# Optimization experiments

Hardware: AMD Instinct MI355X
Metric: run time of the kernel (lower is better)

The kernel has to match this reference:

```python
import jax, jax.numpy as jnp
import numpy as np

B, S, D, H = 4, 2048, 1024, 16
HD = D // H  # head_dim = 64


def setup_inputs() -> dict:
    key = jax.random.key(0)
    ks = jax.random.split(key, 9)
    sd = 1.0 / np.sqrt(D)
    x = jax.random.normal(ks[0], (B, S, D), dtype=jnp.float32)
    Wq = jax.random.normal(ks[1], (D, D), dtype=jnp.float32) * sd
    Wk = jax.random.normal(ks[2], (D, D), dtype=jnp.float32) * sd
    Wv = jax.random.normal(ks[3], (D, D), dtype=jnp.float32) * sd
    Wo = jax.random.normal(ks[4], (D, D), dtype=jnp.float32) * sd
    bq = jax.random.normal(ks[5], (D,), dtype=jnp.float32) * sd
    bk = jax.random.normal(ks[6], (D,), dtype=jnp.float32) * sd
    bv = jax.random.normal(ks[7], (D,), dtype=jnp.float32) * sd
    bo = jax.random.normal(ks[8], (D,), dtype=jnp.float32) * sd
    return {"x": x, "Wq": Wq, "bq": bq, "Wk": Wk, "bk": bk,
            "Wv": Wv, "bv": bv, "Wo": Wo, "bo": bo}


def reference(x, Wq, bq, Wk, bk, Wv, bv, Wo, bo):
    b, s, d = x.shape
    scale = jnp.float32(np.sqrt(HD))
    # projections, split into heads: (b, h, s, hd)
    def heads(y):
        return y.reshape(b, s, H, HD).transpose(0, 2, 1, 3)
    Q = heads(x @ Wq + bq)
    K = heads(x @ Wk + bk)
    V = heads(x @ Wv + bv)
    # (b, h, s, s) scores with causal mask
    scores = jnp.einsum('bhqd,bhkd->bhqk', Q, K) / scale
    causal = jnp.tril(jnp.ones((s, s), dtype=bool))
    scores = jnp.where(causal[None, None], scores, jnp.float32(-jnp.inf))
    probs = jax.nn.softmax(scores, axis=-1)
    out = jnp.einsum('bhqk,bhkd->bhqd', probs, V)
    out = out.transpose(0, 2, 1, 3).reshape(b, s, d)
    return out @ Wo + bo
```

## Files before the change

### kernel.cpp

```cpp
#include <hip/hip_runtime.h>
#include <hip/hip_bf16.h>
#include <cstdint>

typedef __bf16 bf16x8 __attribute__((ext_vector_type(8)));
typedef float f32x4 __attribute__((ext_vector_type(4)));
typedef float f32x16 __attribute__((ext_vector_type(16)));
typedef unsigned short u16t;

__device__ __forceinline__ u16t f2bf(float f) {
    uint32_t u = __builtin_bit_cast(uint32_t, f);
    u += 0x7FFF + ((u >> 16) & 1);
    return (u16t)(u >> 16);
}

constexpr int Bb = 4, Ss = 2048, Dd = 1024, Hh = 16;
constexpr int Mrows = Bb * Ss;
constexpr float NEG = -1e30f;
constexpr float QSCALE = 0.125f * 1.44269504088896340736f;

__global__ __launch_bounds__(256) void cvt_bf16(const float* __restrict__ in,
                                                u16t* __restrict__ out, int n) {
    int i = (blockIdx.x * 256 + threadIdx.x) * 4;
    if (i >= n) return;
    float4 v = *(const float4*)(in + i);
    u16t o[4] = {f2bf(v.x), f2bf(v.y), f2bf(v.z), f2bf(v.w)};
    *(ushort4*)(out + i) = *(ushort4*)o;
}

__global__ __launch_bounds__(256) void transpose_cvt4(const float* __restrict__ W0,
                                                      const float* __restrict__ W1,
                                                      const float* __restrict__ W2,
                                                      const float* __restrict__ W3,
                                                      u16t* __restrict__ Tqkv,
                                                      u16t* __restrict__ To) {
    __shared__ float tile[64][65];
    int z = blockIdx.z;
    const float* W = z == 0 ? W0 : z == 1 ? W1 : z == 2 ? W2 : W3;
    u16t* WT = z < 3 ? Tqkv + (size_t)z * Dd * Dd : To;
    int n0 = blockIdx.x * 64, k0 = blockIdx.y * 64;
    int c = threadIdx.x & 63, r0 = (threadIdx.x >> 6) * 16;
    for (int i = 0; i < 16; i++)
        tile[c][r0 + i] = W[(size_t)(k0 + r0 + i) * Dd + n0 + c];
    __syncthreads();
    for (int i = 0; i < 16; i++)
        WT[(size_t)(n0 + r0 + i) * Dd + k0 + c] = f2bf(tile[r0 + i][c]);
}

__global__ __launch_bounds__(256) void gemm_qkv(const u16t* __restrict__ A,
                                                const u16t* __restrict__ BT,
                                                const float* __restrict__ bq,
                                                const float* __restrict__ bk,
                                                const float* __restrict__ bvv,
                                                u16t* __restrict__ Qh,
                                                u16t* __restrict__ Kh,
                                                u16t* __restrict__ Vt) {
    __shared__ __align__(16) u16t Asm[128 * 32];
    __shared__ __align__(16) u16t Bsm[128 * 32];
    int tid = threadIdx.x, lane = tid & 63, w = tid >> 6;
    int wm = w >> 1, wn = w & 1;
    int ln = lane & 15, g = lane >> 4;
    int bid = blockIdx.x;
    int wg = (bid & 7) * 192 + (bid >> 3);
    int n0 = (wg % 24) * 128, m0 = (wg / 24) * 128;

    f32x4 acc[4][4] = {};

    int sr = w * 32 + (lane >> 2);
    int sc = (((lane & 3) ^ (sr & 3)) * 8);
    const u16t* Ag0 = A + (size_t)(m0 + sr) * Dd + sc;
    const u16t* Ag1 = A + (size_t)(m0 + sr + 16) * Dd + sc;
    const u16t* Bg0 = BT + (size_t)(n0 + sr) * Dd + sc;
    const u16t* Bg1 = BT + (size_t)(n0 + sr + 16) * Dd + sc;
    u16t* As0 = &Asm[(w * 32) * 32];
    u16t* As1 = &Asm[(w * 32 + 16) * 32];
    u16t* Bs0 = &Bsm[(w * 32) * 32];
    u16t* Bs1 = &Bsm[(w * 32 + 16) * 32];

    for (int k0 = 0; k0 < Dd; k0 += 32) {
        __syncthreads();
        __builtin_amdgcn_global_load_lds(Ag0 + k0, As0, 16, 0, 0);
        __builtin_amdgcn_global_load_lds(Ag1 + k0, As1, 16, 0, 0);
        __builtin_amdgcn_global_load_lds(Bg0 + k0, Bs0, 16, 0, 0);
        __builtin_amdgcn_global_load_lds(Bg1 + k0, Bs1, 16, 0, 0);
        __syncthreads();
        bf16x8 af[4], bf[4];
        #pragma unroll
        for (int i = 0; i < 4; i++) {
            int row = wm * 64 + i * 16 + ln;
            af[i] = *(const bf16x8*)&Asm[row * 32 + ((g ^ (row & 3)) * 8)];
        }
        #pragma unroll
        for (int j = 0; j < 4; j++) {
            int row = wn * 64 + j * 16 + ln;
            bf[j] = *(const bf16x8*)&Bsm[row * 32 + ((g ^ (row & 3)) * 8)];
        }
        #pragma unroll
        for (int i = 0; i < 4; i++)
            #pragma unroll
            for (int j = 0; j < 4; j++)
                acc[i][j] = __builtin_amdgcn_mfma_f32_16x16x32_bf16(af[i], bf[j], acc[i][j], 0, 0, 0);
    }

    #pragma unroll
    for (int i = 0; i < 4; i++) {
        #pragma unroll
        for (int j = 0; j < 4; j++) {
            int col = n0 + wn * 64 + j * 16 + ln;
            int seg = col >> 10, c1k = col & 1023;
            float bias = seg == 0 ? bq[c1k] : seg == 1 ? bk[c1k] : bvv[c1k];
            int rowb = m0 + wm * 64 + i * 16 + g * 4;
            int b = rowb >> 11, s = rowb & 2047, h = c1k >> 6, hd = c1k & 63;
            if (seg == 0) {
                for (int r = 0; r < 4; r++) {
                    float v = (acc[i][j][r] + bias) * QSCALE;
                    Qh[((size_t)(b * Hh + h) * Ss + s + r) * 64 + hd] = f2bf(v);
                }
            } else if (seg == 1) {
                for (int r = 0; r < 4; r++)
                    Kh[((size_t)(b * Hh + h) * Ss + s + r) * 64 + hd] = f2bf(acc[i][j][r] + bias);
            } else {
                u16t pk4[4];
                for (int r = 0; r < 4; r++) pk4[r] = f2bf(acc[i][j][r] + bias);
                *(ushort4*)(Vt + ((size_t)((b * Hh + h) * 64 + hd) << 11) + s) = *(ushort4*)pk4;
            }
        }
    }
}

__global__ __launch_bounds__(256) void gemm_o(const u16t* __restrict__ A,
                                              const u16t* __restrict__ BT,
                                              const float* __restrict__ bias,
                                              float* __restrict__ outF) {
    __shared__ __align__(16) u16t Asm[128 * 32];
    __shared__ __align__(16) u16t Bsm[128 * 32];
    int tid = threadIdx.x, lane = tid & 63, w = tid >> 6;
    int wm = w >> 1, wn = w & 1;
    int ln = lane & 15, g = lane >> 4;
    int bid = blockIdx.x;
    int wg = (bid & 7) * 64 + (bid >> 3);
    int n0 = (wg & 7) * 128, m0 = (wg >> 3) * 128;

    f32x4 acc[4][4] = {};

    int sr = w * 32 + (lane >> 2);
    int sc = (((lane & 3) ^ (sr & 3)) * 8);
    const u16t* Ag0 = A + (size_t)(m0 + sr) * Dd + sc;
    const u16t* Ag1 = A + (size_t)(m0 + sr + 16) * Dd + sc;
    const u16t* Bg0 = BT + (size_t)(n0 + sr) * Dd + sc;
    const u16t* Bg1 = BT + (size_t)(n0 + sr + 16) * Dd + sc;
    u16t* As0 = &Asm[(w * 32) * 32];
    u16t* As1 = &Asm[(w * 32 + 16) * 32];
    u16t* Bs0 = &Bsm[(w * 32) * 32];
    u16t* Bs1 = &Bsm[(w * 32 + 16) * 32];

    for (int k0 = 0; k0 < Dd; k0 += 32) {
        __syncthreads();
        __builtin_amdgcn_global_load_lds(Ag0 + k0, As0, 16, 0, 0);
        __builtin_amdgcn_global_load_lds(Ag1 + k0, As1, 16, 0, 0);
        __builtin_amdgcn_global_load_lds(Bg0 + k0, Bs0, 16, 0, 0);
        __builtin_amdgcn_global_load_lds(Bg1 + k0, Bs1, 16, 0, 0);
        __syncthreads();
        bf16x8 af[4], bf[4];
        #pragma unroll
        for (int i = 0; i < 4; i++) {
            int row = wm * 64 + i * 16 + ln;
            af[i] = *(const bf16x8*)&Asm[row * 32 + ((g ^ (row & 3)) * 8)];
        }
        #pragma unroll
        for (int j = 0; j < 4; j++) {
            int row = wn * 64 + j * 16 + ln;
            bf[j] = *(const bf16x8*)&Bsm[row * 32 + ((g ^ (row & 3)) * 8)];
        }
        #pragma unroll
        for (int i = 0; i < 4; i++)
            #pragma unroll
            for (int j = 0; j < 4; j++)
                acc[i][j] = __builtin_amdgcn_mfma_f32_16x16x32_bf16(af[i], bf[j], acc[i][j], 0, 0, 0);
    }

    #pragma unroll
    for (int i = 0; i < 4; i++) {
        #pragma unroll
        for (int j = 0; j < 4; j++) {
            int col = n0 + wn * 64 + j * 16 + ln;
            float bv = bias[col];
            int rowb = m0 + wm * 64 + i * 16 + g * 4;
            for (int r = 0; r < 4; r++)
                outF[(size_t)(rowb + r) * Dd + col] = acc[i][j][r] + bv;
        }
    }
}

__global__ __launch_bounds__(256) void attn(const u16t* __restrict__ Qh,
                                            const u16t* __restrict__ Kh,
                                            const u16t* __restrict__ Vt,
                                            u16t* __restrict__ Ob) {
    __shared__ __align__(16) u16t Ksm[2][64 * 64];
    __shared__ __align__(16) u16t Vsm[2][64 * 64];

    int tid = threadIdx.x, lane = tid & 63, w = tid >> 6;
    int l31 = lane & 31, hi = lane >> 5;
    int flat = blockIdx.y * 8 + blockIdx.x;
    int xcd = flat & 7, jj = flat >> 3;
    int bh = xcd * 8 + (jj >> 3);
    int ip = jj & 7;

    const u16t* Kb = Kh + (size_t)bh * Ss * 64;
    const u16t* Vb = Vt + (size_t)bh * 64 * Ss;

    int sr0 = w * 16 + (lane >> 3);
    int sr1 = sr0 + 8;
    int sc0 = (((lane & 7) ^ (sr0 & 7) ^ ((sr0 >> 3) & 3)) * 8);
    int sc1 = (((lane & 7) ^ (sr1 & 7) ^ ((sr1 >> 3) & 3)) * 8);
    const u16t* Kg0 = Kb + (size_t)sr0 * 64 + sc0;
    const u16t* Kg1 = Kb + (size_t)sr1 * 64 + sc1;
    const u16t* Vg0 = Vb + (size_t)sr0 * Ss + sc0;
    const u16t* Vg1 = Vb + (size_t)sr1 * Ss + sc1;

    auto stage = [&](int buf, int t) {
        size_t koff = (size_t)t * 64 * 64;
        size_t voff = (size_t)t * 64;
        __builtin_amdgcn_global_load_lds(Kg0 + koff, &Ksm[buf][(w * 2 + 0) * 512], 16, 0, 0);
        __builtin_amdgcn_global_load_lds(Kg1 + koff, &Ksm[buf][(w * 2 + 1) * 512], 16, 0, 0);
        __builtin_amdgcn_global_load_lds(Vg0 + voff, &Vsm[buf][(w * 2 + 0) * 512], 16, 0, 0);
        __builtin_amdgcn_global_load_lds(Vg1 + voff, &Vsm[buf][(w * 2 + 1) * 512], 16, 0, 0);
    };

    int swzr = (l31 & 7) ^ ((l31 >> 3) & 3);

    for (int task = 0; task < 2; task++) {
        int qx = task == 0 ? ip : 15 - ip;
        int qb = qx * 128;
        int q0w = qb + w * 32;
        int qlane = q0w + l31;

        bf16x8 qB[4];
        {
            const u16t* Qp = Qh + ((size_t)bh * Ss + qlane) * 64 + hi * 8;
            #pragma unroll
            for (int ks = 0; ks < 4; ks++)
                qB[ks] = *(const bf16x8*)(Qp + 16 * ks);
        }

        f32x16 oacc[2] = {};
        float m_run = NEG, l_run = 0.f;
        int nt = (qb >> 6) + 2;

        stage(0, 0);
        __syncthreads();

        for (int t = 0; t < nt; t++) {
            int cur = t & 1;
            int kv0 = t << 6;
            if (t + 1 < nt) stage(cur ^ 1, t + 1);

            bool active = (kv0 <= q0w + 31);
            if (active) {
                f32x16 p0 = {}, p1 = {};
                __builtin_amdgcn_s_setprio(1);
                #pragma unroll
                for (int ks = 0; ks < 4; ks++) {
                    int cc = (2 * ks + hi) ^ swzr;
                    bf16x8 ka0 = *(const bf16x8*)&Ksm[cur][(size_t)l31 * 64 + cc * 8];
                    bf16x8 ka1 = *(const bf16x8*)&Ksm[cur][(size_t)(32 + l31) * 64 + cc * 8];
                    p0 = __builtin_amdgcn_mfma_f32_32x32x16_bf16(ka0, qB[ks], p0, 0, 0, 0);
                    p1 = __builtin_amdgcn_mfma_f32_32x32x16_bf16(ka1, qB[ks], p1, 0, 0, 0);
                }
                __builtin_amdgcn_s_setprio(0);

                if (kv0 + 63 > q0w) {
                    #pragma unroll
                    for (int r = 0; r < 16; r++) {
                        int kvg = kv0 + (r & 3) + 8 * (r >> 2) + 4 * hi;
                        if (kvg > qlane)      p0[r] = NEG;
                        if (kvg + 32 > qlane) p1[r] = NEG;
                    }
                }

                float ma = fmaxf(p0[0], p1[0]), mb = fmaxf(p0[1], p1[1]);
                float mc = fmaxf(p0[2], p1[2]), md = fmaxf(p0[3], p1[3]);
                #pragma unroll
                for (int r = 4; r < 16; r += 4) {
                    ma = fmaxf(ma, fmaxf(p0[r], p1[r]));
                    mb = fmaxf(mb, fmaxf(p0[r + 1], p1[r + 1]));
                    mc = fmaxf(mc, fmaxf(p0[r + 2], p1[r + 2]));
                    md = fmaxf(md, fmaxf(p0[r + 3], p1[r + 3]));
                }
                float mt = fmaxf(fmaxf(ma, mb), fmaxf(mc, md));
                mt = fmaxf(mt, __shfl_xor(mt, 32));
                if (__any(mt > m_run + 10.0f)) {
                    float mn = fmaxf(m_run, mt);
                    float al = __builtin_exp2f(m_run - mn);
                    m_run = mn;
                    l_run *= al;
                    #pragma unroll
                    for (int r = 0; r < 16; r++) { oacc[0][r] *= al; oacc[1][r] *= al; }
                }
                #pragma unroll
                for (int r = 0; r < 16; r++) {
                    p0[r] = __builtin_exp2f(p0[r] - m_run);
                    p1[r] = __builtin_exp2f(p1[r] - m_run);
                }
                float sa = 0.f, sb = 0.f, sc2 = 0.f, sd = 0.f;
                #pragma unroll
                for (int r = 0; r < 16; r += 4) {
                    sa += p0[r] + p1[r];
                    sb += p0[r + 1] + p1[r + 1];
                    sc2 += p0[r + 2] + p1[r + 2];
                    sd += p0[r + 3] + p1[r + 3];
                }
                float rsum = (sa + sb) + (sc2 + sd);
                rsum += __shfl_xor(rsum, 32);
                l_run += rsum;

                bf16x8 pb[4];
                {
                    uint32_t c0, c1, c2, c3;
                    asm("v_cvt_pk_bf16_f32 %0, %1, %2" : "=v"(c0) : "v"(p0[0]), "v"(p0[1]));
                    asm("v_cvt_pk_bf16_f32 %0, %1, %2" : "=v"(c1) : "v"(p0[2]), "v"(p0[3]));
                    asm("v_cvt_pk_bf16_f32 %0, %1, %2" : "=v"(c2) : "v"(p0[4]), "v"(p0[5]));
                    asm("v_cvt_pk_bf16_f32 %0, %1, %2" : "=v"(c3) : "v"(p0[6]), "v"(p0[7]));
                    asm volatile("v_permlane32_swap_b32 %0, %1" : "+v"(c0), "+v"(c2));
                    asm volatile("v_permlane32_swap_b32 %0, %1" : "+v"(c1), "+v"(c3));
                    uint32_t w4[4] = {c0, c1, c2, c3};
                    pb[0] = *(bf16x8*)w4;
                    uint32_t d0, d1, d2, d3;
                    asm("v_cvt_pk_bf16_f32 %0, %1, %2" : "=v"(d0) : "v"(p0[8]),  "v"(p0[9]));
                    asm("v_cvt_pk_bf16_f32 %0, %1, %2" : "=v"(d1) : "v"(p0[10]), "v"(p0[11]));
                    asm("v_cvt_pk_bf16_f32 %0, %1, %2" : "=v"(d2) : "v"(p0[12]), "v"(p0[13]));
                    asm("v_cvt_pk_bf16_f32 %0, %1, %2" : "=v"(d3) : "v"(p0[14]), "v"(p0[15]));
                    asm volatile("v_permlane32_swap_b32 %0, %1" : "+v"(d0), "+v"(d2));
                    asm volatile("v_permlane32_swap_b32 %0, %1" : "+v"(d1), "+v"(d3));
                    uint32_t w5[4] = {d0, d1, d2, d3};
                    pb[1] = *(bf16x8*)w5;
                    uint32_t e0, e1, e2, e3;
                    asm("v_cvt_pk_bf16_f32 %0, %1, %2" : "=v"(e0) : "v"(p1[0]), "v"(p1[1]));
                    asm("v_cvt_pk_bf16_f32 %0, %1, %2" : "=v"(e1) : "v"(p1[2]), "v"(p1[3]));
                    asm("v_cvt_pk_bf16_f32 %0, %1, %2" : "=v"(e2) : "v"(p1[4]), "v"(p1[5]));
                    asm("v_cvt_pk_bf16_f32 %0, %1, %2" : "=v"(e3) : "v"(p1[6]), "v"(p1[7]));
                    asm volatile("v_permlane32_swap_b32 %0, %1" : "+v"(e0), "+v"(e2));
                    asm volatile("v_permlane32_swap_b32 %0, %1" : "+v"(e1), "+v"(e3));
                    uint32_t w6[4] = {e0, e1, e2, e3};
                    pb[2] = *(bf16x8*)w6;
                    uint32_t f0, f1, f2, f3;
                    asm("v_cvt_pk_bf16_f32 %0, %1, %2" : "=v"(f0) : "v"(p1[8]),  "v"(p1[9]));
                    asm("v_cvt_pk_bf16_f32 %0, %1, %2" : "=v"(f1) : "v"(p1[10]), "v"(p1[11]));
                    asm("v_cvt_pk_bf16_f32 %0, %1, %2" : "=v"(f2) : "v"(p1[12]), "v"(p1[13]));
                    asm("v_cvt_pk_bf16_f32 %0, %1, %2" : "=v"(f3) : "v"(p1[14]), "v"(p1[15]));
                    asm volatile("v_permlane32_swap_b32 %0, %1" : "+v"(f0), "+v"(f2));
                    asm volatile("v_permlane32_swap_b32 %0, %1" : "+v"(f1), "+v"(f3));
                    uint32_t w7[4] = {f0, f1, f2, f3};
                    pb[3] = *(bf16x8*)w7;
                }

                __builtin_amdgcn_s_setprio(1);
                #pragma unroll
                for (int dt = 0; dt < 2; dt++) {
                    int drow = dt * 32 + l31;
                    #pragma unroll
                    for (int ks = 0; ks < 4; ks++) {
                        int cc = (2 * ks + hi) ^ swzr;
                        bf16x8 va = *(const bf16x8*)&Vsm[cur][(size_t)drow * 64 + cc * 8];
                        oacc[dt] = __builtin_amdgcn_mfma_f32_32x32x16_bf16(va, pb[ks], oacc[dt], 0, 0, 0);
                    }
                }
                __builtin_amdgcn_s_setprio(0);
            }
            __syncthreads();
        }

        float inv = 1.0f / l_run;
        int b = bh >> 4, h = bh & 15;
        u16t* Op = Ob + ((size_t)(b * Ss + qlane)) * Dd + h * 64;
        #pragma unroll
        for (int dt = 0; dt < 2; dt++)
            #pragma unroll
            for (int rq = 0; rq < 4; rq++) {
                u16t pk4[4];
                #pragma unroll
                for (int j = 0; j < 4; j++) pk4[j] = f2bf(oacc[dt][rq * 4 + j] * inv);
                int d0 = dt * 32 + rq * 8 + hi * 4;
                *(ushort4*)(Op + d0) = *(ushort4*)pk4;
            }
    }
}

extern "C" void kernel_launch(void* const* d_in, const int* in_sizes, int n_in,
                              void* d_out, int out_size, void* d_ws, size_t ws_size,
                              hipStream_t stream) {
    const float* x  = (const float*)d_in[0];
    const float* Wq = (const float*)d_in[1];
    const float* bq = (const float*)d_in[2];
    const float* Wk = (const float*)d_in[3];
    const float* bk = (const float*)d_in[4];
    const float* Wv = (const float*)d_in[5];
    const float* bv = (const float*)d_in[6];
    const float* Wo = (const float*)d_in[7];
    const float* bo = (const float*)d_in[8];

    char* ws = (char*)d_ws;
    size_t off = 0;
    auto alloc = [&](size_t bytes) { char* p = ws + off; off += (bytes + 255) & ~(size_t)255; return p; };
    u16t* xb    = (u16t*)alloc((size_t)Mrows * Dd * 2);
    u16t* WqkvT = (u16t*)alloc((size_t)3 * Dd * Dd * 2);
    u16t* WoT   = (u16t*)alloc((size_t)Dd * Dd * 2);
    u16t* Qh    = (u16t*)alloc((size_t)Mrows * Dd * 2);
    u16t* Kh    = (u16t*)alloc((size_t)Mrows * Dd * 2);
    u16t* Vtp   = (u16t*)alloc((size_t)Mrows * Dd * 2);
    u16t* Ob    = (u16t*)alloc((size_t)Mrows * Dd * 2);

    int nx = Mrows * Dd;
    cvt_bf16<<<nx / (256 * 4), 256, 0, stream>>>(x, xb, nx);
    dim3 tg(16, 16, 4);
    transpose_cvt4<<<tg, 256, 0, stream>>>(Wq, Wk, Wv, Wo, WqkvT, WoT);

    gemm_qkv<<<1536, 256, 0, stream>>>(xb, WqkvT, bq, bk, bv, Qh, Kh, Vtp);

    dim3 ga(8, Bb * Hh);
    attn<<<ga, 256, 0, stream>>>(Qh, Kh, Vtp, Ob);

    gemm_o<<<512, 256, 0, stream>>>(Ob, WoT, bo, (float*)d_out);
}
```

Measured before the change: 208.4 us.

## Process paired causal query tiles in one KV sweep sharing staged K/V

Each block used to handle its two query tiles (ip and 15-ip) one after the other, loading K/V tiles from global memory for each pass. Now both tiles are processed in a single loop over KV tiles, so every staged K/V tile in LDS serves both query tiles, and the early-tile task skips once it passes its causal limit. The pairing index is also mirrored for half of the blocks to change the XCD/L2 access order. In exchange, two sets of Q fragments and accumulators stay live at once, which raises register pressure and may lower occupancy or cause spills.

```diff
diff --git a/kernel.cpp b/kernel.cpp
--- a/kernel.cpp
+++ b/kernel.cpp
@@ -203,7 +203,9 @@
     int flat = blockIdx.y * 8 + blockIdx.x;
     int xcd = flat & 7, jj = flat >> 3;
     int bh = xcd * 8 + (jj >> 3);
-    int ip = jj & 7;
+    int ipb = jj & 7;
+    int ip = ((jj >> 5) & 1) ? 7 - ipb : ipb;
+    int qxA = ip, qxB = 15 - ip;
 
     const u16t* Kb = Kh + (size_t)bh * Ss * 64;
     const u16t* Vb = Vt + (size_t)bh * 64 * Ss;
@@ -228,157 +230,174 @@
 
     int swzr = (l31 & 7) ^ ((l31 >> 3) & 3);
 
-    for (int task = 0; task < 2; task++) {
-        int qx = task == 0 ? ip : 15 - ip;
-        int qb = qx * 128;
-        int q0w = qb + w * 32;
-        int qlane = q0w + l31;
-
-        bf16x8 qB[4];
+    auto body = [&](const bf16x8* qB, float& m_run, float& l_run, f32x16* oacc,
+                    int q0w, int qlane, int kv0, int cur) {
+        f32x16 p0 = {}, p1 = {};
+        __builtin_amdgcn_s_setprio(1);
+        #pragma unroll
+        for (int ks = 0; ks < 4; ks++) {
+            int cc = (2 * ks + hi) ^ swzr;
+            bf16x8 ka0 = *(const bf16x8*)&Ksm[cur][(size_t)l31 * 64 + cc * 8];
+            bf16x8 ka1 = *(const bf16x8*)&Ksm[cur][(size_t)(32 + l31) * 64 + cc * 8];
+            p0 = __builtin_amdgcn_mfma_f32_32x32x16_bf16(ka0, qB[ks], p0, 0, 0, 0);
+            p1 = __builtin_amdgcn_mfma_f32_32x32x16_bf16(ka1, qB[ks], p1, 0, 0, 0);
+        }
+        __builtin_amdgcn_s_setprio(0);
+
+        if (kv0 + 63 > q0w) {
+            #pragma unroll
+            for (int r = 0; r < 16; r++) {
+                int kvg = kv0 + (r & 3) + 8 * (r >> 2) + 4 * hi;
+                if (kvg > qlane)      p0[r] = NEG;
+                if (kvg + 32 > qlane) p1[r] = NEG;
+            }
+        }
+
+        float ma = fmaxf(p0[0], p1[0]), mb = fmaxf(p0[1], p1[1]);
+        float mc = fmaxf(p0[2], p1[2]), md = fmaxf(p0[3], p1[3]);
+        #pragma unroll
+        for (int r = 4; r < 16; r += 4) {
+            ma = fmaxf(ma, fmaxf(p0[r], p1[r]));
+            mb = fmaxf(mb, fmaxf(p0[r + 1], p1[r + 1]));
+            mc = fmaxf(mc, fmaxf(p0[r + 2], p1[r + 2]));
+            md = fmaxf(md, fmaxf(p0[r + 3], p1[r + 3]));
+        }
+        float mt = fmaxf(fmaxf(ma, mb), fmaxf(mc, md));
+        mt = fmaxf(mt, __shfl_xor(mt, 32));
+        if (__any(mt > m_run + 10.0f)) {
+            float mn = fmaxf(m_run, mt);
+            float al = __builtin_exp2f(m_run - mn);
+            m_run = mn;
+            l_run *= al;
+            #pragma unroll
+            for (int r = 0; r < 16; r++) { oacc[0][r] *= al; oacc[1][r] *= al; }
+        }
+        #pragma unroll
+        for (int r = 0; r < 16; r++) {
+            p0[r] = __builtin_exp2f(p0[r] - m_run);
+            p1[r] = __builtin_exp2f(p1[r] - m_run);
+        }
+        float sa = 0.f, sb = 0.f, sc2 = 0.f, sd = 0.f;
+        #pragma unroll
+        for (int r = 0; r < 16; r += 4) {
+            sa += p0[r] + p1[r];
+            sb += p0[r + 1] + p1[r + 1];
+            sc2 += p0[r + 2] + p1[r + 2];
+            sd += p0[r + 3] + p1[r + 3];
+        }
+        float rsum = (sa + sb) + (sc2 + sd);
+        rsum += __shfl_xor(rsum, 32);
+        l_run += rsum;
+
+        bf16x8 pb[4];
         {
-            const u16t* Qp = Qh + ((size_t)bh * Ss + qlane) * 64 + hi * 8;
-            #pragma unroll
-            for (int ks = 0; ks < 4; ks++)
-                qB[ks] = *(const bf16x8*)(Qp + 16 * ks);
-        }
-
-        f32x16 oacc[2] = {};
-        float m_run = NEG, l_run = 0.f;
-        int nt = (qb >> 6) + 2;
-
-        stage(0, 0);
+            uint32_t c0, c1, c2, c3;
+            asm("v_cvt_pk_bf16_f32 %0, %1, %2" : "=v"(c0) : "v"(p0[0]), "v"(p0[1]));
+            asm("v_cvt_pk_bf16_f32 %0, %1, %2" : "=v"(c1) : "v"(p0[2]), "v"(p0[3]));
+            asm("v_cvt_pk_bf16_f32 %0, %1, %2" : "=v"(c2) : "v"(p0[4]), "v"(p0[5]));
+            asm("v_cvt_pk_bf16_f32 %0, %1, %2" : "=v"(c3) : "v"(p0[6]), "v"(p0[7]));
+            asm volatile("v_permlane32_swap_b32 %0, %1" : "+v"(c0), "+v"(c2));
+            asm volatile("v_permlane32_swap_b32 %0, %1" : "+v"(c1), "+v"(c3));
+            uint32_t w4[4] = {c0, c1, c2, c3};
+            pb[0] = *(bf16x8*)w4;
+            uint32_t d0, d1, d2, d3;
+            asm("v_cvt_pk_bf16_f32 %0, %1, %2" : "=v"(d0) : "v"(p0[8]),  "v"(p0[9]));
+            asm("v_cvt_pk_bf16_f32 %0, %1, %2" : "=v"(d1) : "v"(p0[10]), "v"(p0[11]));
+            asm("v_cvt_pk_bf16_f32 %0, %1, %2" : "=v"(d2) : "v"(p0[12]), "v"(p0[13]));
+            asm("v_cvt_pk_bf16_f32 %0, %1, %2" : "=v"(d3) : "v"(p0[14]), "v"(p0[15]));
+            asm volatile("v_permlane32_swap_b32 %0, %1" : "+v"(d0), "+v"(d2));
+            asm volatile("v_permlane32_swap_b32 %0, %1" : "+v"(d1), "+v"(d3));
+            uint32_t w5[4] = {d0, d1, d2, d3};
+            pb[1] = *(bf16x8*)w5;
+            uint32_t e0, e1, e2, e3;
+            asm("v_cvt_pk_bf16_f32 %0, %1, %2" : "=v"(e0) : "v"(p1[0]), "v"(p1[1]));
+            asm("v_cvt_pk_bf16_f32 %0, %1, %2" : "=v"(e1) : "v"(p1[2]), "v"(p1[3]));
+            asm("v_cvt_pk_bf16_f32 %0, %1, %2" : "=v"(e2) : "v"(p1[4]), "v"(p1[5]));
+            asm("v_cvt_pk_bf16_f32 %0, %1, %2" : "=v"(e3) : "v"(p1[6]), "v"(p1[7]));
+            asm volatile("v_permlane32_swap_b32 %0, %1" : "+v"(e0), "+v"(e2));
+            asm volatile("v_permlane32_swap_b32 %0, %1" : "+v"(e1), "+v"(e3));
+            uint32_t w6[4] = {e0, e1, e2, e3};
+            pb[2] = *(bf16x8*)w6;
+            uint32_t f0, f1, f2, f3;
+            asm("v_cvt_pk_bf16_f32 %0, %1, %2" : "=v"(f0) : "v"(p1[8]),  "v"(p1[9]));
+            asm("v_cvt_pk_bf16_f32 %0, %1, %2" : "=v"(f1) : "v"(p1[10]), "v"(p1[11]));
+            asm("v_cvt_pk_bf16_f32 %0, %1, %2" : "=v"(f2) : "v"(p1[12]), "v"(p1[13]));
+            asm("v_cvt_pk_bf16_f32 %0, %1, %2" : "=v"(f3) : "v"(p1[14]), "v"(p1[15]));
+            asm volatile("v_permlane32_swap_b32 %0, %1" : "+v"(f0), "+v"(f2));
+            asm volatile("v_permlane32_swap_b32 %0, %1" : "+v"(f1), "+v"(f3));
+            uint32_t w7[4] = {f0, f1, f2, f3};
+            pb[3] = *(bf16x8*)w7;
+        }
+
+        __builtin_amdgcn_s_setprio(1);
+        #pragma unroll
+        for (int dt = 0; dt < 2; dt++) {
+            int drow = dt * 32 + l31;
+            #pragma unroll
+            for (int ks = 0; ks < 4; ks++) {
+                int cc = (2 * ks + hi) ^ swzr;
+                bf16x8 va = *(const bf16x8*)&Vsm[cur][(size_t)drow * 64 + cc * 8];
+                oacc[dt] = __builtin_amdgcn_mfma_f32_32x32x16_bf16(va, pb[ks], oacc[dt], 0, 0, 0);
+            }
+        }
+        __builtin_amdgcn_s_setprio(0);
+    };
+
+    int q0wA = qxA * 128 + w * 32, qlaneA = q0wA + l31;
+    int q0wB = qxB * 128 + w * 32, qlaneB = q0wB + l31;
+    bf16x8 qBA[4], qBB[4];
+    {
+        const u16t* QpA = Qh + ((size_t)bh * Ss + qlaneA) * 64 + hi * 8;
+        const u16t* QpB = Qh + ((size_t)bh * Ss + qlaneB) * 64 + hi * 8;
+        #pragma unroll
+        for (int ks = 0; ks < 4; ks++) {
+            qBA[ks] = *(const bf16x8*)(QpA + 16 * ks);
+            qBB[ks] = *(const bf16x8*)(QpB + 16 * ks);
+        }
+    }
+    f32x16 oaccA[2] = {}, oaccB[2] = {};
+    float mA = NEG, lA = 0.f, mB = NEG, lB = 0.f;
+
+    int ntB = 2 * qxB + 2;
+
+    stage(0, 0);
+    __syncthreads();
+
+    for (int t = 0; t < ntB; t++) {
+        int cur = t & 1;
+        int kv0 = t << 6;
+        if (t + 1 < ntB) stage(cur ^ 1, t + 1);
+
+        if (kv0 <= q0wA + 31) body(qBA, mA, lA, oaccA, q0wA, qlaneA, kv0, cur);
+        if (kv0 <= q0wB + 31) body(qBB, mB, lB, oaccB, q0wB, qlaneB, kv0, cur);
         __syncthreads();
-
-        for (int t = 0; t < nt; t++) {
-            int cur = t & 1;
-            int kv0 = t << 6;
-            if (t + 1 < nt) stage(cur ^ 1, t + 1);
-
-            bool active = (kv0 <= q0w + 31);
-            if (active) {
-                f32x16 p0 = {}, p1 = {};
-                __builtin_amdgcn_s_setprio(1);
-                #pragma unroll
-                for (int ks = 0; ks < 4; ks++) {
-                    int cc = (2 * ks + hi) ^ swzr;
-                    bf16x8 ka0 = *(const bf16x8*)&Ksm[cur][(size_t)l31 * 64 + cc * 8];
-                    bf16x8 ka1 = *(const bf16x8*)&Ksm[cur][(size_t)(32 + l31) * 64 + cc * 8];
-                    p0 = __builtin_amdgcn_mfma_f32_32x32x16_bf16(ka0, qB[ks], p0, 0, 0, 0);
-                    p1 = __builtin_amdgcn_mfma_f32_32x32x16_bf16(ka1, qB[ks], p1, 0, 0, 0);
-                }
-                __builtin_amdgcn_s_setprio(0);
-
-                if (kv0 + 63 > q0w) {
-                    #pragma unroll
-                    for (int r = 0; r < 16; r++) {
-                        int kvg = kv0 + (r & 3) + 8 * (r >> 2) + 4 * hi;
-                        if (kvg > qlane)      p0[r] = NEG;
-                        if (kvg + 32 > qlane) p1[r] = NEG;
-                    }
-                }
-
-                float ma = fmaxf(p0[0], p1[0]), mb = fmaxf(p0[1], p1[1]);
-                float mc = fmaxf(p0[2], p1[2]), md = fmaxf(p0[3], p1[3]);
-                #pragma unroll
-                for (int r = 4; r < 16; r += 4) {
-                    ma = fmaxf(ma, fmaxf(p0[r], p1[r]));
-                    mb = fmaxf(mb, fmaxf(p0[r + 1], p1[r + 1]));
-                    mc = fmaxf(mc, fmaxf(p0[r + 2], p1[r + 2]));
-                    md = fmaxf(md, fmaxf(p0[r + 3], p1[r + 3]));
-                }
-                float mt = fmaxf(fmaxf(ma, mb), fmaxf(mc, md));
-                mt = fmaxf(mt, __shfl_xor(mt, 32));
-                if (__any(mt > m_run + 10.0f)) {
-                    float mn = fmaxf(m_run, mt);
-                    float al = __builtin_exp2f(m_run - mn);
-                    m_run = mn;
-                    l_run *= al;
-                    #pragma unroll
-                    for (int r = 0; r < 16; r++) { oacc[0][r] *= al; oacc[1][r] *= al; }
-                }
-                #pragma unroll
-                for (int r = 0; r < 16; r++) {
-                    p0[r] = __builtin_exp2f(p0[r] - m_run);
-                    p1[r] = __builtin_exp2f(p1[r] - m_run);
-                }
-                float sa = 0.f, sb = 0.f, sc2 = 0.f, sd = 0.f;
-                #pragma unroll
-                for (int r = 0; r < 16; r += 4) {
-                    sa += p0[r] + p1[r];
-                    sb += p0[r + 1] + p1[r + 1];
-                    sc2 += p0[r + 2] + p1[r + 2];
-                    sd += p0[r + 3] + p1[r + 3];
-                }
-                float rsum = (sa + sb) + (sc2 + sd);
-                rsum += __shfl_xor(rsum, 32);
-                l_run += rsum;
-
-                bf16x8 pb[4];
-                {
-                    uint32_t c0, c1, c2, c3;
-                    asm("v_cvt_pk_bf16_f32 %0, %1, %2" : "=v"(c0) : "v"(p0[0]), "v"(p0[1]));
-                    asm("v_cvt_pk_bf16_f32 %0, %1, %2" : "=v"(c1) : "v"(p0[2]), "v"(p0[3]));
-                    asm("v_cvt_pk_bf16_f32 %0, %1, %2" : "=v"(c2) : "v"(p0[4]), "v"(p0[5]));
-                    asm("v_cvt_pk_bf16_f32 %0, %1, %2" : "=v"(c3) : "v"(p0[6]), "v"(p0[7]));
-                    asm volatile("v_permlane32_swap_b32 %0, %1" : "+v"(c0), "+v"(c2));
-                    asm volatile("v_permlane32_swap_b32 %0, %1" : "+v"(c1), "+v"(c3));
-                    uint32_t w4[4] = {c0, c1, c2, c3};
-                    pb[0] = *(bf16x8*)w4;
-                    uint32_t d0, d1, d2, d3;
-                    asm("v_cvt_pk_bf16_f32 %0, %1, %2" : "=v"(d0) : "v"(p0[8]),  "v"(p0[9]));
-                    asm("v_cvt_pk_bf16_f32 %0, %1, %2" : "=v"(d1) : "v"(p0[10]), "v"(p0[11]));
-                    asm("v_cvt_pk_bf16_f32 %0, %1, %2" : "=v"(d2) : "v"(p0[12]), "v"(p0[13]));
-                    asm("v_cvt_pk_bf16_f32 %0, %1, %2" : "=v"(d3) : "v"(p0[14]), "v"(p0[15]));
-                    asm volatile("v_permlane32_swap_b32 %0, %1" : "+v"(d0), "+v"(d2));
-                    asm volatile("v_permlane32_swap_b32 %0, %1" : "+v"(d1), "+v"(d3));
-                    uint32_t w5[4] = {d0, d1, d2, d3};
-                    pb[1] = *(bf16x8*)w5;
-                    uint32_t e0, e1, e2, e3;
-                    asm("v_cvt_pk_bf16_f32 %0, %1, %2" : "=v"(e0) : "v"(p1[0]), "v"(p1[1]));
-                    asm("v_cvt_pk_bf16_f32 %0, %1, %2" : "=v"(e1) : "v"(p1[2]), "v"(p1[3]));
-                    asm("v_cvt_pk_bf16_f32 %0, %1, %2" : "=v"(e2) : "v"(p1[4]), "v"(p1[5]));
-                    asm("v_cvt_pk_bf16_f32 %0, %1, %2" : "=v"(e3) : "v"(p1[6]), "v"(p1[7]));
-                    asm volatile("v_permlane32_swap_b32 %0, %1" : "+v"(e0), "+v"(e2));
-                    asm volatile("v_permlane32_swap_b32 %0, %1" : "+v"(e1), "+v"(e3));
-                    uint32_t w6[4] = {e0, e1, e2, e3};
-                    pb[2] = *(bf16x8*)w6;
-                    uint32_t f0, f1, f2, f3;
-                    asm("v_cvt_pk_bf16_f32 %0, %1, %2" : "=v"(f0) : "v"(p1[8]),  "v"(p1[9]));
-                    asm("v_cvt_pk_bf16_f32 %0, %1, %2" : "=v"(f1) : "v"(p1[10]), "v"(p1[11]));
-                    asm("v_cvt_pk_bf16_f32 %0, %1, %2" : "=v"(f2) : "v"(p1[12]), "v"(p1[13]));
-                    asm("v_cvt_pk_bf16_f32 %0, %1, %2" : "=v"(f3) : "v"(p1[14]), "v"(p1[15]));
-                    asm volatile("v_permlane32_swap_b32 %0, %1" : "+v"(f0), "+v"(f2));
-                    asm volatile("v_permlane32_swap_b32 %0, %1" : "+v"(f1), "+v"(f3));
-                    uint32_t w7[4] = {f0, f1, f2, f3};
-                    pb[3] = *(bf16x8*)w7;
-                }
-
-                __builtin_amdgcn_s_setprio(1);
-                #pragma unroll
-                for (int dt = 0; dt < 2; dt++) {
-                    int drow = dt * 32 + l31;
-                    #pragma unroll
-                    for (int ks = 0; ks < 4; ks++) {
-                        int cc = (2 * ks + hi) ^ swzr;
-                        bf16x8 va = *(const bf16x8*)&Vsm[cur][(size_t)drow * 64 + cc * 8];
-                        oacc[dt] = __builtin_amdgcn_mfma_f32_32x32x16_bf16(va, pb[ks], oacc[dt], 0, 0, 0);
-                    }
-                }
-                __builtin_amdgcn_s_setprio(0);
-            }
-            __syncthreads();
-        }
-
-        float inv = 1.0f / l_run;
-        int b = bh >> 4, h = bh & 15;
-        u16t* Op = Ob + ((size_t)(b * Ss + qlane)) * Dd + h * 64;
+    }
+
+    int b = bh >> 4, h = bh & 15;
+    {
+        float inv = 1.0f / lA;
+        u16t* Op = Ob + ((size_t)(b * Ss + qlaneA)) * Dd + h * 64;
         #pragma unroll
         for (int dt = 0; dt < 2; dt++)
             #pragma unroll
             for (int rq = 0; rq < 4; rq++) {
                 u16t pk4[4];
                 #pragma unroll
-                for (int j = 0; j < 4; j++) pk4[j] = f2bf(oacc[dt][rq * 4 + j] * inv);
+                for (int j = 0; j < 4; j++) pk4[j] = f2bf(oaccA[dt][rq * 4 + j] * inv);
+                int d0 = dt * 32 + rq * 8 + hi * 4;
+                *(ushort4*)(Op + d0) = *(ushort4*)pk4;
+            }
+    }
+    {
+        float inv = 1.0f / lB;
+        u16t* Op = Ob + ((size_t)(b * Ss + qlaneB)) * Dd + h * 64;
+        #pragma unroll
+        for (int dt = 0; dt < 2; dt++)
+            #pragma unroll
+            for (int rq = 0; rq < 4; rq++) {
+                u16t pk4[4];
+                #pragma unroll
+                for (int j = 0; j < 4; j++) pk4[j] = f2bf(oaccB[dt][rq * 4 + j] * inv);
                 int d0 = dt * 32 + rq * 8 + hi * 4;
                 *(ushort4*)(Op + d0) = *(ushort4*)pk4;
             }
```

Result: slower. 213.0 us (+2.2%).

## Use 128x256 GEMM tiles with 8 waves and triple-buffered async LDS loads

Applied to the files above, without the earlier changes.

Replaces the QKV and output-projection GEMM main loops with a shared macro. Each 512-thread block computes a 128x256 tile with BK=64. The global-to-LDS loads are triple-buffered, using explicit s_barrier and vmcnt waits so the next tiles load while the current one is computed. This aims to hide memory latency and halve the barrier count per K step, at the cost of more LDS per block (about 144KB), which limits occupancy to one block per CU. The hand-counted vmcnt values must match the per-thread load count exactly.

```diff
diff --git a/kernel.cpp b/kernel.cpp
--- a/kernel.cpp
+++ b/kernel.cpp
@@ -46,7 +46,80 @@
         WT[(size_t)(n0 + r0 + i) * Dd + k0 + c] = f2bf(tile[r0 + i][c]);
 }
 
-__global__ __launch_bounds__(256) void gemm_qkv(const u16t* __restrict__ A,
+
+#define GEMM_CORE_512(A_, BT_, m0_, n0_)                                                    \
+    __shared__ __align__(16) u16t Asm3[3][128 * 64];                                        \
+    __shared__ __align__(16) u16t Bsm3[3][256 * 64];                                        \
+    int tid = threadIdx.x, lane = tid & 63, w = tid >> 6;                                   \
+    int wm = w >> 2, wn = w & 3;                                                            \
+    int ln = lane & 15, g = lane >> 4;                                                      \
+    int l3 = lane >> 3, l7 = lane & 7;                                                      \
+    int swz = (l7 ^ (l3 & 7)) * 8;                                                          \
+    const u16t* Ap[2]; int Ao[2];                                                           \
+    _Pragma("unroll")                                                                       \
+    for (int ii = 0; ii < 2; ii++) {                                                        \
+        int rg = m0_ + ii * 64 + w * 8 + l3;                                                \
+        Ap[ii] = A_ + (size_t)rg * Dd + swz;                                                \
+        Ao[ii] = ii * 4096 + w * 512;                                                       \
+    }                                                                                       \
+    const u16t* Bp[4]; int Bo[4];                                                           \
+    _Pragma("unroll")                                                                       \
+    for (int ii = 0; ii < 4; ii++) {                                                        \
+        int rg = n0_ + ii * 64 + w * 8 + l3;                                                \
+        Bp[ii] = BT_ + (size_t)rg * Dd + swz;                                               \
+        Bo[ii] = ii * 4096 + w * 512;                                                       \
+    }                                                                                       \
+    auto stage = [&](int buf, int t) {                                                      \
+        int k0 = t * 64;                                                                    \
+        _Pragma("unroll")                                                                   \
+        for (int ii = 0; ii < 2; ii++)                                                      \
+            __builtin_amdgcn_global_load_lds(Ap[ii] + k0, &Asm3[buf][Ao[ii]], 16, 0, 0);    \
+        _Pragma("unroll")                                                                   \
+        for (int ii = 0; ii < 4; ii++)                                                      \
+            __builtin_amdgcn_global_load_lds(Bp[ii] + k0, &Bsm3[buf][Bo[ii]], 16, 0, 0);    \
+    };                                                                                      \
+    f32x4 acc[4][4] = {};                                                                   \
+    int coff[2] = {((g) ^ (ln & 7)) * 8, ((4 + g) ^ (ln & 7)) * 8};                         \
+    int arow = wm * 64 + ln;                                                                \
+    int brow = wn * 64 + ln;                                                                \
+    auto compute = [&](int buf) {                                                           \
+        bf16x8 af[4][2], bfr[4][2];                                                         \
+        _Pragma("unroll")                                                                   \
+        for (int i = 0; i < 4; i++)                                                         \
+            _Pragma("unroll")                                                               \
+            for (int ks = 0; ks < 2; ks++)                                                  \
+                af[i][ks] = *(const bf16x8*)&Asm3[buf][(arow + i * 16) * 64 + coff[ks]];    \
+        _Pragma("unroll")                                                                   \
+        for (int j = 0; j < 4; j++)                                                         \
+            _Pragma("unroll")                                                               \
+            for (int ks = 0; ks < 2; ks++)                                                  \
+                bfr[j][ks] = *(const bf16x8*)&Bsm3[buf][(brow + j * 16) * 64 + coff[ks]];   \
+        _Pragma("unroll")                                                                   \
+        for (int i = 0; i < 4; i++)                                                         \
+            _Pragma("unroll")                                                               \
+            for (int j = 0; j < 4; j++) {                                                   \
+                acc[i][j] = __builtin_amdgcn_mfma_f32_16x16x32_bf16(af[i][0], bfr[j][0],    \
+                                                                    acc[i][j], 0, 0, 0);    \
+                acc[i][j] = __builtin_amdgcn_mfma_f32_16x16x32_bf16(af[i][1], bfr[j][1],    \
+                                                                    acc[i][j], 0, 0, 0);    \
+            }                                                                               \
+    };                                                                                      \
+    stage(0, 0);                                                                            \
+    stage(1, 1);                                                                            \
+    for (int t = 0; t < 14; t++) {                                                          \
+        asm volatile("s_barrier" ::: "memory");                                             \
+        stage((t + 2) % 3, t + 2);                                                          \
+        asm volatile("s_waitcnt vmcnt(12)" ::: "memory");                                   \
+        compute(t % 3);                                                                     \
+    }                                                                                       \
+    asm volatile("s_barrier" ::: "memory");                                                 \
+    asm volatile("s_waitcnt vmcnt(6)" ::: "memory");                                        \
+    compute(14 % 3);                                                                        \
+    asm volatile("s_barrier" ::: "memory");                                                 \
+    asm volatile("s_waitcnt vmcnt(0)" ::: "memory");                                        \
+    compute(15 % 3);
+
+__global__ __launch_bounds__(512) void gemm_qkv(const u16t* __restrict__ A,
                                                 const u16t* __restrict__ BT,
                                                 const float* __restrict__ bq,
                                                 const float* __restrict__ bk,
@@ -54,52 +127,11 @@
                                                 u16t* __restrict__ Qh,
                                                 u16t* __restrict__ Kh,
                                                 u16t* __restrict__ Vt) {
-    __shared__ __align__(16) u16t Asm[128 * 32];
-    __shared__ __align__(16) u16t Bsm[128 * 32];
-    int tid = threadIdx.x, lane = tid & 63, w = tid >> 6;
-    int wm = w >> 1, wn = w & 1;
-    int ln = lane & 15, g = lane >> 4;
     int bid = blockIdx.x;
-    int wg = (bid & 7) * 192 + (bid >> 3);
-    int n0 = (wg % 24) * 128, m0 = (wg / 24) * 128;
-
-    f32x4 acc[4][4] = {};
-
-    int sr = w * 32 + (lane >> 2);
-    int sc = (((lane & 3) ^ (sr & 3)) * 8);
-    const u16t* Ag0 = A + (size_t)(m0 + sr) * Dd + sc;
-    const u16t* Ag1 = A + (size_t)(m0 + sr + 16) * Dd + sc;
-    const u16t* Bg0 = BT + (size_t)(n0 + sr) * Dd + sc;
-    const u16t* Bg1 = BT + (size_t)(n0 + sr + 16) * Dd + sc;
-    u16t* As0 = &Asm[(w * 32) * 32];
-    u16t* As1 = &Asm[(w * 32 + 16) * 32];
-    u16t* Bs0 = &Bsm[(w * 32) * 32];
-    u16t* Bs1 = &Bsm[(w * 32 + 16) * 32];
-
-    for (int k0 = 0; k0 < Dd; k0 += 32) {
-        __syncthreads();
-        __builtin_amdgcn_global_load_lds(Ag0 + k0, As0, 16, 0, 0);
-        __builtin_amdgcn_global_load_lds(Ag1 + k0, As1, 16, 0, 0);
-        __builtin_amdgcn_global_load_lds(Bg0 + k0, Bs0, 16, 0, 0);
-        __builtin_amdgcn_global_load_lds(Bg1 + k0, Bs1, 16, 0, 0);
-        __syncthreads();
-        bf16x8 af[4], bf[4];
-        #pragma unroll
-        for (int i = 0; i < 4; i++) {
-            int row = wm * 64 + i * 16 + ln;
-            af[i] = *(const bf16x8*)&Asm[row * 32 + ((g ^ (row & 3)) * 8)];
-        }
-        #pragma unroll
-        for (int j = 0; j < 4; j++) {
-            int row = wn * 64 + j * 16 + ln;
-            bf[j] = *(const bf16x8*)&Bsm[row * 32 + ((g ^ (row & 3)) * 8)];
-        }
-        #pragma unroll
-        for (int i = 0; i < 4; i++)
-            #pragma unroll
-            for (int j = 0; j < 4; j++)
-                acc[i][j] = __builtin_amdgcn_mfma_f32_16x16x32_bf16(af[i], bf[j], acc[i][j], 0, 0, 0);
-    }
+    int wg = (bid & 7) * 96 + (bid >> 3);
+    int m0 = (wg / 12) * 128, n0 = (wg % 12) * 256;
+
+    GEMM_CORE_512(A, BT, m0, n0)
 
     #pragma unroll
     for (int i = 0; i < 4; i++) {
@@ -127,56 +159,15 @@
     }
 }
 
-__global__ __launch_bounds__(256) void gemm_o(const u16t* __restrict__ A,
+__global__ __launch_bounds__(512) void gemm_o(const u16t* __restrict__ A,
                                               const u16t* __restrict__ BT,
                                               const float* __restrict__ bias,
                                               float* __restrict__ outF) {
-    __shared__ __align__(16) u16t Asm[128 * 32];
-    __shared__ __align__(16) u16t Bsm[128 * 32];
-    int tid = threadIdx.x, lane = tid & 63, w = tid >> 6;
-    int wm = w >> 1, wn = w & 1;
-    int ln = lane & 15, g = lane >> 4;
     int bid = blockIdx.x;
-    int wg = (bid & 7) * 64 + (bid >> 3);
-    int n0 = (wg & 7) * 128, m0 = (wg >> 3) * 128;
-
-    f32x4 acc[4][4] = {};
-
-    int sr = w * 32 + (lane >> 2);
-    int sc = (((lane & 3) ^ (sr & 3)) * 8);
-    const u16t* Ag0 = A + (size_t)(m0 + sr) * Dd + sc;
-    const u16t* Ag1 = A + (size_t)(m0 + sr + 16) * Dd + sc;
-    const u16t* Bg0 = BT + (size_t)(n0 + sr) * Dd + sc;
-    const u16t* Bg1 = BT + (size_t)(n0 + sr + 16) * Dd + sc;
-    u16t* As0 = &Asm[(w * 32) * 32];
-    u16t* As1 = &Asm[(w * 32 + 16) * 32];
-    u16t* Bs0 = &Bsm[(w * 32) * 32];
-    u16t* Bs1 = &Bsm[(w * 32 + 16) * 32];
-
-    for (int k0 = 0; k0 < Dd; k0 += 32) {
-        __syncthreads();
-        __builtin_amdgcn_global_load_lds(Ag0 + k0, As0, 16, 0, 0);
-        __builtin_amdgcn_global_load_lds(Ag1 + k0, As1, 16, 0, 0);
-        __builtin_amdgcn_global_load_lds(Bg0 + k0, Bs0, 16, 0, 0);
-        __builtin_amdgcn_global_load_lds(Bg1 + k0, Bs1, 16, 0, 0);
-        __syncthreads();
-        bf16x8 af[4], bf[4];
-        #pragma unroll
-        for (int i = 0; i < 4; i++) {
-            int row = wm * 64 + i * 16 + ln;
-            af[i] = *(const bf16x8*)&Asm[row * 32 + ((g ^ (row & 3)) * 8)];
-        }
-        #pragma unroll
-        for (int j = 0; j < 4; j++) {
-            int row = wn * 64 + j * 16 + ln;
-            bf[j] = *(const bf16x8*)&Bsm[row * 32 + ((g ^ (row & 3)) * 8)];
-        }
-        #pragma unroll
-        for (int i = 0; i < 4; i++)
-            #pragma unroll
-            for (int j = 0; j < 4; j++)
-                acc[i][j] = __builtin_amdgcn_mfma_f32_16x16x32_bf16(af[i], bf[j], acc[i][j], 0, 0, 0);
-    }
+    int wg = (bid & 7) * 32 + (bid >> 3);
+    int m0 = (wg >> 2) * 128, n0 = (wg & 3) * 256;
+
+    GEMM_CORE_512(A, BT, m0, n0)
 
     #pragma unroll
     for (int i = 0; i < 4; i++) {
@@ -414,10 +405,10 @@
     dim3 tg(16, 16, 4);
     transpose_cvt4<<<tg, 256, 0, stream>>>(Wq, Wk, Wv, Wo, WqkvT, WoT);
 
-    gemm_qkv<<<1536, 256, 0, stream>>>(xb, WqkvT, bq, bk, bv, Qh, Kh, Vtp);
+    gemm_qkv<<<768, 512, 0, stream>>>(xb, WqkvT, bq, bk, bv, Qh, Kh, Vtp);
 
     dim3 ga(8, Bb * Hh);
     attn<<<ga, 256, 0, stream>>>(Qh, Kh, Vtp, Ob);
 
-    gemm_o<<<512, 256, 0, stream>>>(Ob, WoT, bo, (float*)d_out);
-}
+    gemm_o<<<256, 512, 0, stream>>>(Ob, WoT, bo, (float*)d_out);
+}
```

Result: no change. 205.0 us (-1.6%).
